# Optimization experiments

Measured on AMD Instinct MI355X. Metric: run time of the kernel, lower is better.

## Reference

```python
import jax, jax.numpy as jnp
import numpy as np

B, S, HID = 2, 2048, 2048
NH, NKV, HD = 16, 4, 128
MAXPOS = 2048


def _rope_tables(features, length, max_timescale=10000.0):
    fraction = jnp.arange(0, features, 2, dtype=jnp.float32) / features
    inv_freq = 1.0 / (max_timescale ** fraction)
    sinusoid = jnp.einsum('i,j->ij', jnp.arange(length, dtype=jnp.float32), inv_freq)
    sinusoid = jnp.concatenate([sinusoid, sinusoid], axis=-1)  # [length, features]
    return jnp.sin(sinusoid), jnp.cos(sinusoid)


def rotate_half(x):
    x1, x2 = jnp.split(x, 2, axis=-1)
    return jnp.concatenate([-x2, x1], axis=-1)


def setup_inputs() -> dict:
    key = jax.random.key(0)
    k1, k2, k3, k4, k5 = jax.random.split(key, 5)
    scale = 1.0 / np.sqrt(HID)
    hidden_states = jax.random.normal(k1, (B, S, HID), dtype=jnp.float32)
    Wq = jax.random.normal(k2, (NH * HD, HID), dtype=jnp.float32) * scale
    Wk = jax.random.normal(k3, (NKV * HD, HID), dtype=jnp.float32) * scale
    Wv = jax.random.normal(k4, (NKV * HD, HID), dtype=jnp.float32) * scale
    Wo = jax.random.normal(k5, (HID, NH * HD), dtype=jnp.float32) * scale
    # causal additive mask [B,1,S,S]
    neg = jnp.finfo(jnp.float32).min
    causal = jnp.where(jnp.tril(jnp.ones((S, S), dtype=bool)), 0.0, neg)
    attention_mask = jnp.broadcast_to(causal[None, None], (B, 1, S, S))
    sin, cos = _rope_tables(HD, MAXPOS)
    return {"hidden_states": hidden_states, "attention_mask": attention_mask,
            "Wq": Wq, "Wk": Wk, "Wv": Wv, "Wo": Wo, "sin": sin, "cos": cos}


def reference(hidden_states, attention_mask, Wq, Wk, Wv, Wo, sin, cos):
    bsz, qlen, _ = hidden_states.shape
    # projections (Linear, no bias): x @ W.T -> [B,S,heads,hd]
    q = (hidden_states @ Wq.T).reshape(bsz, qlen, NH, HD)
    k = (hidden_states @ Wk.T).reshape(bsz, qlen, NKV, HD)
    v = (hidden_states @ Wv.T).reshape(bsz, qlen, NKV, HD)
    # rotary embedding (applied in [B,S,H,D] layout)
    qcos = cos[:qlen][None, :, None, :]
    qsin = sin[:qlen][None, :, None, :]
    q = q * qcos + rotate_half(q) * qsin
    k = k * qcos + rotate_half(k) * qsin
    # GQA: repeat_kv equivalent via einsum grouping; expand kv heads to NH
    n_rep = NH // NKV
    q_g = q.reshape(bsz, qlen, NKV, n_rep, HD)  # group queries per kv head
    # scores: NOTE original applies no 1/sqrt(d) scaling
    scores = jnp.einsum('bqhrd,bkhd->bhrqk', q_g, k).reshape(bsz, NH, qlen, qlen)
    mask = attention_mask.at[:, :, :, 0].set(0.0)
    scores = scores + mask
    probs = jax.nn.softmax(scores.astype(jnp.float32), axis=-1).astype(q.dtype)
    probs_g = probs.reshape(bsz, NKV, n_rep, qlen, qlen)
    out = jnp.einsum('bhrqk,bkhd->bqhrd', probs_g, v).reshape(bsz, qlen, NH * HD)
    return out @ Wo.T
```

## Files before the change

kernel.cpp:

```cpp
#include <hip/hip_runtime.h>
#include <hip/hip_bf16.h>

typedef _Float16 f16x8 __attribute__((ext_vector_type(8)));
typedef __fp16 h16x2 __attribute__((ext_vector_type(2)));
typedef float f32x4 __attribute__((ext_vector_type(4)));
typedef float f32x16 __attribute__((ext_vector_type(16)));

#define B_    2
#define S_    2048
#define HID_  2048
#define NH_   16
#define NKV_  4
#define HD_   128
#define M_TOK 4096
#define NQKV  3072

#define MFMA16(a, b, c) __builtin_amdgcn_mfma_f32_16x16x32_f16(a, b, c, 0, 0, 0)
#define MFMA32(a, b, c) __builtin_amdgcn_mfma_f32_32x32x16_f16(a, b, c, 0, 0, 0)

union UW { unsigned u; h16x2 h; };

__device__ __forceinline__ unsigned short f2h(float f) {
  _Float16 h = (_Float16)f;
  return *(unsigned short*)&h;
}

__device__ __forceinline__ void gload_lds16(const unsigned short* g, unsigned short* l) {
  __builtin_amdgcn_global_load_lds((const __attribute__((address_space(1))) void*)g,
                                   (__attribute__((address_space(3))) void*)l,
                                   16, 0, 0);
}

__global__ void cast_f32_f16(const float* __restrict__ src, unsigned short* __restrict__ dst, int n4) {
  int i = blockIdx.x * blockDim.x + threadIdx.x;
  int stride = gridDim.x * blockDim.x;
  for (int idx = i; idx < n4; idx += stride) {
    float4 v = reinterpret_cast<const float4*>(src)[idx];
    ushort4 o;
    o.x = f2h(v.x); o.y = f2h(v.y); o.z = f2h(v.z); o.w = f2h(v.w);
    reinterpret_cast<ushort4*>(dst)[idx] = o;
  }
}

#define BM 128
#define BN 128
#define BK 32

template <bool OUT16>
__global__ __launch_bounds__(256) void gemm_bt_f16(
    const unsigned short* __restrict__ A, const unsigned short* __restrict__ Bm,
    void* __restrict__ Cv, int M, int N, int K) {
  __shared__ unsigned short As[BM * BK];
  __shared__ unsigned short Bs[BN * BK];
  const int tid  = threadIdx.x;
  const int lane = tid & 63;
  const int wave = tid >> 6;
  const int nbn  = N / BN;
  const int brow = (blockIdx.x / nbn) * BM;
  const int bcol = (blockIdx.x % nbn) * BN;
  const int wr = (wave >> 1) * 64;
  const int wc = (wave & 1) * 64;

  const int srow = wave * 16 + (lane >> 2);
  const int scol = (lane & 3) * 8;
  const unsigned short* ag = A + (size_t)(brow + srow) * K + scol;
  const unsigned short* bg = Bm + (size_t)(bcol + srow) * K + scol;
  unsigned short* aldsw = As + wave * 512;
  unsigned short* bldsw = Bs + wave * 512;

  f32x4 acc[4][4];
#pragma unroll
  for (int m = 0; m < 4; ++m)
#pragma unroll
    for (int n = 0; n < 4; ++n) acc[m][n] = (f32x4){0.f, 0.f, 0.f, 0.f};

  const int lr = lane & 15;
  const int lg = lane >> 4;

  for (int kt = 0; kt < K; kt += BK) {
    __syncthreads();
    gload_lds16(ag + kt, aldsw);
    gload_lds16(ag + (size_t)64 * K + kt, aldsw + 2048);
    gload_lds16(bg + kt, bldsw);
    gload_lds16(bg + (size_t)64 * K + kt, bldsw + 2048);
    __syncthreads();
    f16x8 af[4], bfr[4];
#pragma unroll
    for (int m = 0; m < 4; ++m)
      af[m] = *reinterpret_cast<const f16x8*>(&As[(wr + m * 16 + lr) * BK + lg * 8]);
#pragma unroll
    for (int n = 0; n < 4; ++n)
      bfr[n] = *reinterpret_cast<const f16x8*>(&Bs[(wc + n * 16 + lr) * BK + lg * 8]);
#pragma unroll
    for (int m = 0; m < 4; ++m)
#pragma unroll
      for (int n = 0; n < 4; ++n)
        acc[m][n] = MFMA16(af[m], bfr[n], acc[m][n]);
  }

#pragma unroll
  for (int m = 0; m < 4; ++m) {
#pragma unroll
    for (int r = 0; r < 4; ++r) {
      int row = brow + wr + m * 16 + lg * 4 + r;
      if (OUT16) {
        unsigned short* cp = (unsigned short*)Cv + (size_t)row * N + bcol + wc + lr;
#pragma unroll
        for (int n = 0; n < 4; ++n) cp[n * 16] = f2h(acc[m][n][r]);
      } else {
        float* cp = (float*)Cv + (size_t)row * N + bcol + wc + lr;
#pragma unroll
        for (int n = 0; n < 4; ++n) cp[n * 16] = acc[m][n][r];
      }
    }
  }
}

__global__ void rope_relayout(const unsigned short* __restrict__ QKV,
                              const float* __restrict__ sin_t, const float* __restrict__ cos_t,
                              unsigned short* __restrict__ Qo, unsigned short* __restrict__ Ko,
                              unsigned short* __restrict__ Vt) {
  int idx = blockIdx.x * blockDim.x + threadIdx.x;
  int d  = idx & 63;
  int t  = idx >> 6;
  int hh = t % 24;
  int bs = t / 24;
  int s  = bs & (S_ - 1);
  int b  = bs >> 11;
  const _Float16* xrow = (const _Float16*)QKV + (size_t)bs * NQKV;
  if (hh < 16) {
    float x0 = (float)xrow[hh * 128 + d], x1 = (float)xrow[hh * 128 + 64 + d];
    float c = cos_t[s * 128 + d], sn = sin_t[s * 128 + d];
    unsigned short* qp = Qo + (((size_t)(b * 16 + hh) * S_) + s) * 128 + d;
    qp[0]  = f2h(x0 * c - x1 * sn);
    qp[64] = f2h(x1 * c + x0 * sn);
  } else if (hh < 20) {
    int kvh = hh - 16;
    float x0 = (float)xrow[2048 + kvh * 128 + d], x1 = (float)xrow[2048 + kvh * 128 + 64 + d];
    float c = cos_t[s * 128 + d], sn = sin_t[s * 128 + d];
    unsigned short* kp = Ko + (((size_t)(b * 4 + kvh) * S_) + s) * 128 + d;
    kp[0]  = f2h(x0 * c - x1 * sn);
    kp[64] = f2h(x1 * c + x0 * sn);
  } else {
    int kvh = hh - 20;
    unsigned short x0 = QKV[(size_t)bs * NQKV + 2560 + kvh * 128 + d];
    unsigned short x1 = QKV[(size_t)bs * NQKV + 2560 + kvh * 128 + 64 + d];
    unsigned short* vp = Vt + ((size_t)(b * 4 + kvh) * 128 + d) * S_ + s;
    vp[0]        = x0;
    vp[64 * S_]  = x1;
  }
}

__global__ __launch_bounds__(256, 2) void flash_attn7(
    const unsigned short* __restrict__ Q, const unsigned short* __restrict__ Kk,
    const unsigned short* __restrict__ Vt, unsigned short* __restrict__ Ao) {
  __shared__ _Float16 Kl[2][64 * 128];
  const int lane = threadIdx.x & 63;
  const int w    = threadIdx.x >> 6;
  const int bh   = blockIdx.x & 31;
  const int bq   = 15 - (int)(blockIdx.x >> 5);
  const int b    = bh >> 4, h = bh & 15, kvh = h >> 2;
  const int q31  = lane & 31;
  const int hi   = lane >> 5;
  const int qb   = bq * 128;
  const int wqb  = qb + w * 32;
  const int qrow = wqb + q31;

  const _Float16* Qp = (const _Float16*)Q + (((size_t)(b * 16 + h) * S_) + qrow) * 128;
  const _Float16* Kp = (const _Float16*)Kk + ((size_t)(b * 4 + kvh) * S_) * 128;
  const _Float16* Vp = (const _Float16*)Vt + ((size_t)(b * 4 + kvh) * 128) * S_;

  f16x8 qf[8];
#pragma unroll
  for (int s = 0; s < 8; ++s) {
    f16x8 t = *reinterpret_cast<const f16x8*>(Qp + s * 16 + hi * 8);
#pragma unroll
    for (int j = 0; j < 8; ++j) t[j] = (_Float16)((float)t[j] * 1.44269504f);
    qf[s] = t;
  }

  f32x16 po0 = {}, po1 = {}, po2 = {}, po3 = {};
  float m = -1e30f, l = 0.f;

  const int krow = (lane >> 4);
  const int wklim = wqb + 32;
  const int nt = qb / 64 + 2;

#define STAGE(K0S, BUF)                                                               \
  {                                                                                   \
    unsigned short* kdst = (unsigned short*)Kl[BUF] + w * 2048;                       \
    _Pragma("unroll") for (int jj = 0; jj < 4; ++jj) {                                \
      const int j = w * 4 + jj;                                                       \
      const int kr = j * 4 + krow;                                                    \
      const int kc = (lane & 15) ^ (kr & 7);                                          \
      gload_lds16((const unsigned short*)(Kp + (size_t)((K0S) + kr) * 128 + kc * 8),  \
                  kdst + jj * 512);                                                   \
    }                                                                                 \
  }

  STAGE(0, 0)
  __syncthreads();

  int cur = 0;
  const int r7 = q31 & 7;
  for (int t = 0; t < nt; ++t) {
    const int k0 = t * 64;
    if (t + 1 < nt) STAGE((t + 1) * 64, cur ^ 1)

    if (k0 < wklim) {
      const _Float16* vb = Vp + (size_t)q31 * S_ + k0 + hi * 8;
      f16x8 vf[16];
#pragma unroll
      for (int s = 0; s < 4; ++s) {
        vf[s]      = *reinterpret_cast<const f16x8*>(vb + s * 16);
        vf[4 + s]  = *reinterpret_cast<const f16x8*>(vb + (size_t)32 * S_ + s * 16);
        vf[8 + s]  = *reinterpret_cast<const f16x8*>(vb + (size_t)64 * S_ + s * 16);
        vf[12 + s] = *reinterpret_cast<const f16x8*>(vb + (size_t)96 * S_ + s * 16);
      }

      f32x16 s0 = {}, s1 = {};
      const _Float16* Kc = Kl[cur];
      __builtin_amdgcn_s_setprio(1);
#pragma unroll
      for (int s = 0; s < 8; ++s) {
        const int cc = (hi + 2 * s) ^ r7;
        f16x8 kf0 = *reinterpret_cast<const f16x8*>(Kc + q31 * 128 + cc * 8);
        f16x8 kf1 = *reinterpret_cast<const f16x8*>(Kc + (q31 + 32) * 128 + cc * 8);
        s0 = MFMA32(kf0, qf[s], s0);
        s1 = MFMA32(kf1, qf[s], s1);
      }
      __builtin_amdgcn_s_setprio(0);

      if (k0 + 63 > wqb) {
        int qrel = qrow - k0 - 4 * hi;
#pragma unroll
        for (int r = 0; r < 16; ++r) {
          int cr = (r & 3) + 8 * (r >> 2);
          if (cr > qrel)      s0[r] = -1e30f;
          if (cr + 32 > qrel) s1[r] = -1e30f;
        }
      }
      float tmx[8];
#pragma unroll
      for (int r = 0; r < 8; ++r)
        tmx[r] = fmaxf(fmaxf(s0[r], s0[r + 8]), fmaxf(s1[r], s1[r + 8]));
#pragma unroll
      for (int d = 4; d > 0; d >>= 1)
#pragma unroll
        for (int r = 0; r < d; ++r) tmx[r] = fmaxf(tmx[r], tmx[r + d]);
      float pmax = fmaxf(tmx[0], __shfl_xor(tmx[0], 32));
      if (__any(pmax > m + 8.0f)) {
        float mn = fmaxf(m, pmax);
        float sc = __builtin_amdgcn_exp2f(m - mn);
        l *= sc;
#pragma unroll
        for (int r = 0; r < 16; ++r) {
          po0[r] *= sc; po1[r] *= sc; po2[r] *= sc; po3[r] *= sc;
        }
        m = mn;
      }
#pragma unroll
      for (int r = 0; r < 16; ++r) s0[r] = __builtin_amdgcn_exp2f(s0[r] - m);
#pragma unroll
      for (int r = 0; r < 16; ++r) s1[r] = __builtin_amdgcn_exp2f(s1[r] - m);
      float u[8];
#pragma unroll
      for (int r = 0; r < 8; ++r)
        u[r] = (s0[r] + s0[r + 8]) + (s1[r] + s1[r + 8]);
#pragma unroll
      for (int d = 4; d > 0; d >>= 1)
#pragma unroll
        for (int r = 0; r < d; ++r) u[r] += u[r + d];
      l += u[0] + __shfl_xor(u[0], 32);

      f16x8 pa[4];
#pragma unroll
      for (int sl = 0; sl < 4; ++sl) {
        f32x16 sv = (sl < 2) ? s0 : s1;
        const int R = (sl & 1) * 8;
        UW w00, w01, w10, w11;
        w00.h = __builtin_amdgcn_cvt_pkrtz(sv[R + 0], sv[R + 1]);
        w01.h = __builtin_amdgcn_cvt_pkrtz(sv[R + 2], sv[R + 3]);
        w10.h = __builtin_amdgcn_cvt_pkrtz(sv[R + 4], sv[R + 5]);
        w11.h = __builtin_amdgcn_cvt_pkrtz(sv[R + 6], sv[R + 7]);
        unsigned x00 = __shfl_xor(w00.u, 32);
        unsigned x01 = __shfl_xor(w01.u, 32);
        unsigned x10 = __shfl_xor(w10.u, 32);
        unsigned x11 = __shfl_xor(w11.u, 32);
        UW W0, W1, W2, W3;
        W0.u = hi ? x10 : w00.u;
        W1.u = hi ? x11 : w01.u;
        W2.u = hi ? w10.u : x00;
        W3.u = hi ? w11.u : x01;
        union { unsigned uu[4]; f16x8 v; } pk;
        pk.uu[0] = W0.u; pk.uu[1] = W1.u; pk.uu[2] = W2.u; pk.uu[3] = W3.u;
        pa[sl] = pk.v;
      }

      __builtin_amdgcn_s_setprio(1);
#pragma unroll
      for (int s = 0; s < 4; ++s) {
        po0 = MFMA32(vf[s], pa[s], po0);
        po1 = MFMA32(vf[4 + s], pa[s], po1);
        po2 = MFMA32(vf[8 + s], pa[s], po2);
        po3 = MFMA32(vf[12 + s], pa[s], po3);
      }
      __builtin_amdgcn_s_setprio(0);
    }

    __syncthreads();
    cur ^= 1;
  }
#undef STAGE

  float inv = 1.0f / l;
  unsigned short* orow = Ao + ((size_t)(b * S_ + qrow)) * 2048 + h * 128;
#define STORE_DB(PO, DB)                                                          \
  {                                                                               \
    _Pragma("unroll") for (int a4 = 0; a4 < 4; ++a4) {                            \
      UW e0, e1;                                                                  \
      e0.h = __builtin_amdgcn_cvt_pkrtz(PO[4 * a4 + 0] * inv, PO[4 * a4 + 1] * inv); \
      e1.h = __builtin_amdgcn_cvt_pkrtz(PO[4 * a4 + 2] * inv, PO[4 * a4 + 3] * inv); \
      unsigned long long pv = ((unsigned long long)e1.u << 32) | e0.u;            \
      *reinterpret_cast<unsigned long long*>(orow + DB * 32 + a4 * 8 + hi * 4) = pv; \
    }                                                                             \
  }
  STORE_DB(po0, 0)
  STORE_DB(po1, 1)
  STORE_DB(po2, 2)
  STORE_DB(po3, 3)
#undef STORE_DB
}

extern "C" void kernel_launch(void* const* d_in, const int* in_sizes, int n_in,
                              void* d_out, int out_size, void* d_ws, size_t ws_size,
                              hipStream_t stream) {
  const float* hs    = (const float*)d_in[0];
  const float* Wq    = (const float*)d_in[2];
  const float* Wk    = (const float*)d_in[3];
  const float* Wv    = (const float*)d_in[4];
  const float* Wo    = (const float*)d_in[5];
  const float* sin_t = (const float*)d_in[6];
  const float* cos_t = (const float*)d_in[7];

  char* ws = (char*)d_ws;
  unsigned short* Xb    = (unsigned short*)ws; ws += (size_t)M_TOK * HID_ * 2;
  unsigned short* Wqkvb = (unsigned short*)ws; ws += (size_t)NQKV * HID_ * 2;
  unsigned short* Wob   = (unsigned short*)ws; ws += (size_t)HID_ * HID_ * 2;
  unsigned short* QKV   = (unsigned short*)ws; ws += (size_t)M_TOK * NQKV * 2;
  unsigned short* Qb    = (unsigned short*)ws; ws += (size_t)B_ * NH_ * S_ * HD_ * 2;
  unsigned short* Kb    = (unsigned short*)ws; ws += (size_t)B_ * NKV_ * S_ * HD_ * 2;
  unsigned short* Vtb   = (unsigned short*)ws; ws += (size_t)B_ * NKV_ * S_ * HD_ * 2;
  unsigned short* Aob   = (unsigned short*)ws; ws += (size_t)M_TOK * HID_ * 2;

  cast_f32_f16<<<2048, 256, 0, stream>>>(hs, Xb, M_TOK * HID_ / 4);
  cast_f32_f16<<<1024, 256, 0, stream>>>(Wq, Wqkvb, 2048 * 2048 / 4);
  cast_f32_f16<<<512,  256, 0, stream>>>(Wk, Wqkvb + 2048 * 2048, 512 * 2048 / 4);
  cast_f32_f16<<<512,  256, 0, stream>>>(Wv, Wqkvb + 2560 * 2048, 512 * 2048 / 4);
  cast_f32_f16<<<1024, 256, 0, stream>>>(Wo, Wob, 2048 * 2048 / 4);

  gemm_bt_f16<true><<<(M_TOK / BM) * (NQKV / BN), 256, 0, stream>>>(Xb, Wqkvb, QKV, M_TOK, NQKV, HID_);

  rope_relayout<<<(B_ * S_ * 24 * 64) / 256, 256, 0, stream>>>(QKV, sin_t, cos_t, Qb, Kb, Vtb);

  flash_attn7<<<512, 256, 0, stream>>>(Qb, Kb, Vtb, Aob);

  gemm_bt_f16<false><<<(M_TOK / BM) * (HID_ / BN), 256, 0, stream>>>(Aob, Wob, d_out, M_TOK, HID_, HID_);
}
```

Before: 283.6 us.

## Stage V tiles through double-buffered LDS and merge weight cast launches

V tiles are now prefetched into a second double-buffered LDS array with async global-to-LDS loads, alongside K. The PV MFMA loop reads them from swizzled LDS instead of issuing direct strided global loads each iteration. The four weight-cast kernels are folded into a single launch. This doubles the attention kernel's LDS footprint, which may limit occupancy, and adds LDS read traffic.

```diff
diff --git a/kernel.cpp b/kernel.cpp
--- a/kernel.cpp
+++ b/kernel.cpp
@@ -36,6 +36,26 @@
   int stride = gridDim.x * blockDim.x;
   for (int idx = i; idx < n4; idx += stride) {
     float4 v = reinterpret_cast<const float4*>(src)[idx];
+    ushort4 o;
+    o.x = f2h(v.x); o.y = f2h(v.y); o.z = f2h(v.z); o.w = f2h(v.w);
+    reinterpret_cast<ushort4*>(dst)[idx] = o;
+  }
+}
+
+__global__ void cast_weights(const float* __restrict__ Wq, const float* __restrict__ Wk,
+                             const float* __restrict__ Wv, const float* __restrict__ Wo,
+                             unsigned short* __restrict__ dst) {
+  const int n1 = 2048 * 2048 / 4, n2 = 512 * 2048 / 4;
+  const int ntot = n1 * 2 + n2 * 2;
+  int i = blockIdx.x * blockDim.x + threadIdx.x;
+  int stride = gridDim.x * blockDim.x;
+  for (int idx = i; idx < ntot; idx += stride) {
+    const float* src; int off;
+    if (idx < n1)                { src = Wq; off = idx; }
+    else if (idx < n1 + n2)      { src = Wk; off = idx - n1; }
+    else if (idx < n1 + 2 * n2)  { src = Wv; off = idx - n1 - n2; }
+    else                         { src = Wo; off = idx - n1 - 2 * n2; }
+    float4 v = reinterpret_cast<const float4*>(src)[off];
     ushort4 o;
     o.x = f2h(v.x); o.y = f2h(v.y); o.z = f2h(v.z); o.w = f2h(v.w);
     reinterpret_cast<ushort4*>(dst)[idx] = o;
@@ -151,10 +171,11 @@
   }
 }
 
-__global__ __launch_bounds__(256, 2) void flash_attn7(
+__global__ __launch_bounds__(256, 2) void flash_attn6(
     const unsigned short* __restrict__ Q, const unsigned short* __restrict__ Kk,
     const unsigned short* __restrict__ Vt, unsigned short* __restrict__ Ao) {
   __shared__ _Float16 Kl[2][64 * 128];
+  __shared__ _Float16 Vl[2][128 * 64];
   const int lane = threadIdx.x & 63;
   const int w    = threadIdx.x >> 6;
   const int bh   = blockIdx.x & 31;
@@ -183,18 +204,24 @@
   float m = -1e30f, l = 0.f;
 
   const int krow = (lane >> 4);
+  const int vrow = (lane >> 3);
   const int wklim = wqb + 32;
   const int nt = qb / 64 + 2;
 
 #define STAGE(K0S, BUF)                                                               \
   {                                                                                   \
     unsigned short* kdst = (unsigned short*)Kl[BUF] + w * 2048;                       \
+    unsigned short* vdst = (unsigned short*)Vl[BUF] + w * 2048;                       \
     _Pragma("unroll") for (int jj = 0; jj < 4; ++jj) {                                \
       const int j = w * 4 + jj;                                                       \
       const int kr = j * 4 + krow;                                                    \
       const int kc = (lane & 15) ^ (kr & 7);                                          \
       gload_lds16((const unsigned short*)(Kp + (size_t)((K0S) + kr) * 128 + kc * 8),  \
                   kdst + jj * 512);                                                   \
+      const int vr = j * 8 + vrow;                                                    \
+      const int vc = (lane & 7) ^ (vr & 7);                                           \
+      gload_lds16((const unsigned short*)(Vp + (size_t)vr * S_ + (K0S) + vc * 8),     \
+                  vdst + jj * 512);                                                   \
     }                                                                                 \
   }
 
@@ -208,16 +235,6 @@
     if (t + 1 < nt) STAGE((t + 1) * 64, cur ^ 1)
 
     if (k0 < wklim) {
-      const _Float16* vb = Vp + (size_t)q31 * S_ + k0 + hi * 8;
-      f16x8 vf[16];
-#pragma unroll
-      for (int s = 0; s < 4; ++s) {
-        vf[s]      = *reinterpret_cast<const f16x8*>(vb + s * 16);
-        vf[4 + s]  = *reinterpret_cast<const f16x8*>(vb + (size_t)32 * S_ + s * 16);
-        vf[8 + s]  = *reinterpret_cast<const f16x8*>(vb + (size_t)64 * S_ + s * 16);
-        vf[12 + s] = *reinterpret_cast<const f16x8*>(vb + (size_t)96 * S_ + s * 16);
-      }
-
       f32x16 s0 = {}, s1 = {};
       const _Float16* Kc = Kl[cur];
       __builtin_amdgcn_s_setprio(1);
@@ -297,13 +314,19 @@
         pa[sl] = pk.v;
       }
 
+      const _Float16* Vc = Vl[cur];
       __builtin_amdgcn_s_setprio(1);
 #pragma unroll
       for (int s = 0; s < 4; ++s) {
-        po0 = MFMA32(vf[s], pa[s], po0);
-        po1 = MFMA32(vf[4 + s], pa[s], po1);
-        po2 = MFMA32(vf[8 + s], pa[s], po2);
-        po3 = MFMA32(vf[12 + s], pa[s], po3);
+        const int cc = (hi + 2 * s) ^ r7;
+        f16x8 vf0 = *reinterpret_cast<const f16x8*>(Vc + q31 * 64 + cc * 8);
+        po0 = MFMA32(vf0, pa[s], po0);
+        f16x8 vf1 = *reinterpret_cast<const f16x8*>(Vc + (q31 + 32) * 64 + cc * 8);
+        po1 = MFMA32(vf1, pa[s], po1);
+        f16x8 vf2 = *reinterpret_cast<const f16x8*>(Vc + (q31 + 64) * 64 + cc * 8);
+        po2 = MFMA32(vf2, pa[s], po2);
+        f16x8 vf3 = *reinterpret_cast<const f16x8*>(Vc + (q31 + 96) * 64 + cc * 8);
+        po3 = MFMA32(vf3, pa[s], po3);
       }
       __builtin_amdgcn_s_setprio(0);
     }
@@ -354,16 +377,13 @@
   unsigned short* Aob   = (unsigned short*)ws; ws += (size_t)M_TOK * HID_ * 2;
 
   cast_f32_f16<<<2048, 256, 0, stream>>>(hs, Xb, M_TOK * HID_ / 4);
-  cast_f32_f16<<<1024, 256, 0, stream>>>(Wq, Wqkvb, 2048 * 2048 / 4);
-  cast_f32_f16<<<512,  256, 0, stream>>>(Wk, Wqkvb + 2048 * 2048, 512 * 2048 / 4);
-  cast_f32_f16<<<512,  256, 0, stream>>>(Wv, Wqkvb + 2560 * 2048, 512 * 2048 / 4);
-  cast_f32_f16<<<1024, 256, 0, stream>>>(Wo, Wob, 2048 * 2048 / 4);
+  cast_weights<<<2048, 256, 0, stream>>>(Wq, Wk, Wv, Wo, Wqkvb);
 
   gemm_bt_f16<true><<<(M_TOK / BM) * (NQKV / BN), 256, 0, stream>>>(Xb, Wqkvb, QKV, M_TOK, NQKV, HID_);
 
   rope_relayout<<<(B_ * S_ * 24 * 64) / 256, 256, 0, stream>>>(QKV, sin_t, cos_t, Qb, Kb, Vtb);
 
-  flash_attn7<<<512, 256, 0, stream>>>(Qb, Kb, Vtb, Aob);
+  flash_attn6<<<512, 256, 0, stream>>>(Qb, Kb, Vtb, Aob);
 
   gemm_bt_f16<false><<<(M_TOK / BM) * (HID_ / BN), 256, 0, stream>>>(Aob, Wob, d_out, M_TOK, HID_, HID_);
 }
```

Result: faster. 248.9 us (-12.2%).
